# Kernel tuning notes

Measured on AMD Instinct MI355X. Metric: run time of the kernel, lower is better.

Reference implementation:

```python
import jax, jax.numpy as jnp
import numpy as np

def setup_inputs() -> dict:
    key = jax.random.key(0)
    ks = jax.random.split(key, 6)
    B, H, Dk, Dv = 128, 16, 128, 128
    return {
        "q": jax.random.normal(ks[0], (B, H, 1, Dk), dtype=jnp.float32),
        "k": jax.random.normal(ks[1], (B, H, 1, Dk), dtype=jnp.float32),
        "v": jax.random.normal(ks[2], (B, H, 1, Dv), dtype=jnp.float32),
        "g": jax.random.uniform(ks[3], (B, H, 1), dtype=jnp.float32),
        "beta": jax.random.uniform(ks[4], (B, H, 1), dtype=jnp.float32),
        "last_recurrent_state": jax.random.normal(ks[5], (B, H, Dk, Dv), dtype=jnp.float32),
    }

def reference(q, k, v, g, beta, last_recurrent_state):
    # q,k: (B,H,1,Dk); v: (B,H,1,Dv); g,beta: (B,H,1); state: (B,H,Dk,Dv)
    q_t = q[:, :, 0, :]                      # (B,H,Dk)
    k_t = k[:, :, 0, :]                      # (B,H,Dk)
    v_t = v[:, :, 0, :]                      # (B,H,Dv)
    decay = jnp.exp(g)[..., None]            # (B,H,1,1)
    state = last_recurrent_state * decay     # (B,H,Dk,Dv)
    kv_mem = jnp.einsum('bhkv,bhk->bhv', state, k_t)   # (B,H,Dv)
    delta = (v_t - kv_mem) * beta            # (B,H,Dv)
    state = state + k_t[..., :, None] * delta[..., None, :]  # outer update
    out = jnp.einsum('bhkv,bhk->bhv', state, q_t)       # (B,H,Dv)
    out = out[:, :, None, :]                 # (B,H,1,Dv)
    return jnp.concatenate([out.reshape(-1), state.reshape(-1)], axis=0)
```

## Files before the change

kernel.cpp:

```cpp
#include <hip/hip_runtime.h>


#define DK 128
#define DV 128
typedef float f4 __attribute__((ext_vector_type(4)));

__global__ __launch_bounds__(256) void s1_cell_kernel(
    const float* __restrict__ q,
    const float* __restrict__ k,
    const float* __restrict__ v,
    const float* __restrict__ g,
    const float* __restrict__ beta,
    const float* __restrict__ S,
    float* __restrict__ out,
    int BH)
{
    const int bh   = blockIdx.x;
    const int w    = threadIdx.x >> 6;
    const int lane = threadIdx.x & 63;
    const int half = lane >> 5;
    const int c0   = (lane & 31) * 4;

    __shared__ float apart[4][DV];
    __shared__ float bpart[4][DV];
    __shared__ float skq[4];

    const size_t stile = (size_t)bh * (DK * DV);
    const float* __restrict__ Sb = S + stile;
    float* __restrict__ oS = out + (size_t)BH * DV + stile;

    const int r0 = 32 * w + half;

    f4 s[16];
    #pragma unroll
    for (int i = 0; i < 16; ++i)
        s[i] = *(const f4*)(Sb + (size_t)(r0 + 2 * i) * DV + c0);

    float kv[16], qv[16];
    #pragma unroll
    for (int i = 0; i < 16; ++i) {
        kv[i] = k[bh * DK + r0 + 2 * i];
        qv[i] = q[bh * DK + r0 + 2 * i];
    }

    const float decay = expf(g[bh]);
    const float bta   = beta[bh];

    f4 a = {0.f, 0.f, 0.f, 0.f};
    f4 b = {0.f, 0.f, 0.f, 0.f};
    float kqp = 0.f;
    #pragma unroll
    for (int i = 0; i < 16; ++i) {
        a   += s[i] * kv[i];
        b   += s[i] * qv[i];
        kqp += kv[i] * qv[i];
    }

    a.x += __shfl_xor(a.x, 32, 64);  a.y += __shfl_xor(a.y, 32, 64);
    a.z += __shfl_xor(a.z, 32, 64);  a.w += __shfl_xor(a.w, 32, 64);
    b.x += __shfl_xor(b.x, 32, 64);  b.y += __shfl_xor(b.y, 32, 64);
    b.z += __shfl_xor(b.z, 32, 64);  b.w += __shfl_xor(b.w, 32, 64);
    kqp += __shfl_xor(kqp, 32, 64);

    if (lane < 32) {
        *(f4*)&apart[w][c0] = a;
        *(f4*)&bpart[w][c0] = b;
        if (lane == 0) skq[w] = kqp;
    }
    __syncthreads();

    f4 A  = *(const f4*)&apart[0][c0];
    f4 Bq = *(const f4*)&bpart[0][c0];
    #pragma unroll
    for (int j = 1; j < 4; ++j) {
        A  += *(const f4*)&apart[j][c0];
        Bq += *(const f4*)&bpart[j][c0];
    }
    const float kq = skq[0] + skq[1] + skq[2] + skq[3];

    const f4 vv  = *(const f4*)(v + bh * DV + c0);
    const f4 dlt = (vv - decay * A) * bta;

    if (w == 0 && lane < 32)
        *(f4*)(out + (size_t)bh * DV + c0) = decay * Bq + kq * dlt;

    #pragma unroll
    for (int i = 0; i < 16; ++i) {
        const f4 wr = decay * s[i] + kv[i] * dlt;
        __builtin_nontemporal_store(wr,
            (f4*)(oS + (size_t)(r0 + 2 * i) * DV + c0));
    }
}

extern "C" void kernel_launch(void* const* d_in, const int* in_sizes, int n_in,
                              void* d_out, int out_size, void* d_ws, size_t ws_size,
                              hipStream_t stream) {
    const float* q    = (const float*)d_in[0];
    const float* k    = (const float*)d_in[1];
    const float* v    = (const float*)d_in[2];
    const float* g    = (const float*)d_in[3];
    const float* beta = (const float*)d_in[4];
    const float* S    = (const float*)d_in[5];
    float* out = (float*)d_out;

    const int BH = in_sizes[3];

    s1_cell_kernel<<<BH, 256, 0, stream>>>(q, k, v, g, beta, S, out, BH);
}
```

Before: 249.3 us.

## Split fused delta-rule kernel into reduction pass and grid-stride state rewrite

The single per-head kernel is split in two. The first kernel computes the reductions and writes out, delta and decay, saving delta and decay into global scratch arrays. The second kernel is a flat grid-stride streaming kernel that rereads the state and writes the updated state. This decouples the state write from the register-heavy reduction block so the write streams with a simple access pattern. The cost is a second full read of the state, which may be partly served from cache, plus an extra launch and a fixed BH_MAX limit on the scratch buffers.

```diff
diff --git a/kernel.cpp b/kernel.cpp
--- a/kernel.cpp
+++ b/kernel.cpp
@@ -3,17 +3,20 @@
 
 #define DK 128
 #define DV 128
+#define BH_MAX 2048
 typedef float f4 __attribute__((ext_vector_type(4)));
 
-__global__ __launch_bounds__(256) void s1_cell_kernel(
+__device__ float g_delta[BH_MAX * DV];
+__device__ float g_decay[BH_MAX];
+
+__global__ __launch_bounds__(256) void s1_reduce_kernel(
     const float* __restrict__ q,
     const float* __restrict__ k,
     const float* __restrict__ v,
     const float* __restrict__ g,
     const float* __restrict__ beta,
     const float* __restrict__ S,
-    float* __restrict__ out,
-    int BH)
+    float* __restrict__ out)
 {
     const int bh   = blockIdx.x;
     const int w    = threadIdx.x >> 6;
@@ -25,10 +28,7 @@
     __shared__ float bpart[4][DV];
     __shared__ float skq[4];
 
-    const size_t stile = (size_t)bh * (DK * DV);
-    const float* __restrict__ Sb = S + stile;
-    float* __restrict__ oS = out + (size_t)BH * DV + stile;
-
+    const float* __restrict__ Sb = S + (size_t)bh * (DK * DV);
     const int r0 = 32 * w + half;
 
     f4 s[16];
@@ -69,26 +69,46 @@
     }
     __syncthreads();
 
-    f4 A  = *(const f4*)&apart[0][c0];
-    f4 Bq = *(const f4*)&bpart[0][c0];
-    #pragma unroll
-    for (int j = 1; j < 4; ++j) {
-        A  += *(const f4*)&apart[j][c0];
-        Bq += *(const f4*)&bpart[j][c0];
+    if (w == 0 && lane < 32) {
+        f4 A  = *(const f4*)&apart[0][c0];
+        f4 Bq = *(const f4*)&bpart[0][c0];
+        #pragma unroll
+        for (int j = 1; j < 4; ++j) {
+            A  += *(const f4*)&apart[j][c0];
+            Bq += *(const f4*)&bpart[j][c0];
+        }
+        const float kq = skq[0] + skq[1] + skq[2] + skq[3];
+
+        const f4 vv  = *(const f4*)(v + bh * DV + c0);
+        const f4 dlt = (vv - decay * A) * bta;
+
+        *(f4*)(g_delta + (size_t)bh * DV + c0) = dlt;
+        *(f4*)(out + (size_t)bh * DV + c0)     = decay * Bq + kq * dlt;
+        if (lane == 0) g_decay[bh] = decay;
     }
-    const float kq = skq[0] + skq[1] + skq[2] + skq[3];
+}
 
-    const f4 vv  = *(const f4*)(v + bh * DV + c0);
-    const f4 dlt = (vv - decay * A) * bta;
+__global__ __launch_bounds__(256) void s1_rewrite_kernel(
+    const float* __restrict__ k,
+    const float* __restrict__ S,
+    float* __restrict__ outS,
+    size_t total_f4)
+{
+    const size_t stride = (size_t)gridDim.x * blockDim.x;
+    size_t idx = (size_t)blockIdx.x * blockDim.x + threadIdx.x;
 
-    if (w == 0 && lane < 32)
-        *(f4*)(out + (size_t)bh * DV + c0) = decay * Bq + kq * dlt;
+    const int rem = (int)(idx & 4095);
+    const int row = rem >> 5;
+    const int vc  = (rem & 31) * 4;
 
-    #pragma unroll
-    for (int i = 0; i < 16; ++i) {
-        const f4 wr = decay * s[i] + kv[i] * dlt;
-        __builtin_nontemporal_store(wr,
-            (f4*)(oS + (size_t)(r0 + 2 * i) * DV + c0));
+    for (; idx < total_f4; idx += stride) {
+        const int bh = (int)(idx >> 12);
+        const f4    s   = *(const f4*)(S + (idx << 2));
+        const float dec = g_decay[bh];
+        const float kvv = k[bh * DK + row];
+        const f4    dlt = *(const f4*)(g_delta + (size_t)bh * DV + vc);
+        __builtin_nontemporal_store(dec * s + kvv * dlt,
+                                    (f4*)(outS + (idx << 2)));
     }
 }
 
@@ -105,5 +125,10 @@
 
     const int BH = in_sizes[3];
 
-    s1_cell_kernel<<<BH, 256, 0, stream>>>(q, k, v, g, beta, S, out, BH);
+    s1_reduce_kernel<<<BH, 256, 0, stream>>>(q, k, v, g, beta, S, out);
+
+    const size_t total_f4 = (size_t)BH * (DK * DV / 4);
+    s1_rewrite_kernel<<<4096, 256, 0, stream>>>(k, S,
+                                                out + (size_t)BH * DV,
+                                                total_f4);
 }
```

Result: slower. 261.9 us (+5.0%).

## Process two heads per block, prefetching second state tile during first writeback

Applied to the files above, without the earlier changes.

Each block now handles two (batch,head) tiles, with the grid halved. The second tile's state is loaded before the first tile's results are written back, so the load overlaps the store. State loads become nontemporal and the state stores switch from nontemporal to regular. This doubles register pressure (two 16xf4 arrays), which may lower occupancy, and it adds an extra barrier.

```diff
diff --git a/kernel.cpp b/kernel.cpp
--- a/kernel.cpp
+++ b/kernel.cpp
@@ -15,53 +15,49 @@
     float* __restrict__ out,
     int BH)
 {
-    const int bh   = blockIdx.x;
     const int w    = threadIdx.x >> 6;
     const int lane = threadIdx.x & 63;
     const int half = lane >> 5;
     const int c0   = (lane & 31) * 4;
+    const int r0   = 32 * w + half;
 
     __shared__ float apart[4][DV];
     __shared__ float bpart[4][DV];
     __shared__ float skq[4];
 
-    const size_t stile = (size_t)bh * (DK * DV);
-    const float* __restrict__ Sb = S + stile;
-    float* __restrict__ oS = out + (size_t)BH * DV + stile;
+    const int bh0 = blockIdx.x;
+    const int bh1 = blockIdx.x + gridDim.x;
 
-    const int r0 = 32 * w + half;
-
-    f4 s[16];
+    const float* __restrict__ Sb0 = S + (size_t)bh0 * (DK * DV);
+    f4 s0[16];
     #pragma unroll
     for (int i = 0; i < 16; ++i)
-        s[i] = *(const f4*)(Sb + (size_t)(r0 + 2 * i) * DV + c0);
+        s0[i] = __builtin_nontemporal_load(
+                    (const f4*)(Sb0 + (size_t)(r0 + 2 * i) * DV + c0));
 
-    float kv[16], qv[16];
+    float kv0[16];
     #pragma unroll
-    for (int i = 0; i < 16; ++i) {
-        kv[i] = k[bh * DK + r0 + 2 * i];
-        qv[i] = q[bh * DK + r0 + 2 * i];
-    }
+    for (int i = 0; i < 16; ++i)
+        kv0[i] = k[bh0 * DK + r0 + 2 * i];
 
-    const float decay = expf(g[bh]);
-    const float bta   = beta[bh];
+    const float dec0 = expf(g[bh0]);
+    const float bt0  = beta[bh0];
 
     f4 a = {0.f, 0.f, 0.f, 0.f};
     f4 b = {0.f, 0.f, 0.f, 0.f};
     float kqp = 0.f;
     #pragma unroll
     for (int i = 0; i < 16; ++i) {
-        a   += s[i] * kv[i];
-        b   += s[i] * qv[i];
-        kqp += kv[i] * qv[i];
+        const float qv = q[bh0 * DK + r0 + 2 * i];
+        a   += s0[i] * kv0[i];
+        b   += s0[i] * qv;
+        kqp += kv0[i] * qv;
     }
-
     a.x += __shfl_xor(a.x, 32, 64);  a.y += __shfl_xor(a.y, 32, 64);
     a.z += __shfl_xor(a.z, 32, 64);  a.w += __shfl_xor(a.w, 32, 64);
     b.x += __shfl_xor(b.x, 32, 64);  b.y += __shfl_xor(b.y, 32, 64);
     b.z += __shfl_xor(b.z, 32, 64);  b.w += __shfl_xor(b.w, 32, 64);
     kqp += __shfl_xor(kqp, 32, 64);
-
     if (lane < 32) {
         *(f4*)&apart[w][c0] = a;
         *(f4*)&bpart[w][c0] = b;
@@ -76,20 +72,80 @@
         A  += *(const f4*)&apart[j][c0];
         Bq += *(const f4*)&bpart[j][c0];
     }
-    const float kq = skq[0] + skq[1] + skq[2] + skq[3];
+    const float kq0 = skq[0] + skq[1] + skq[2] + skq[3];
+    const f4 vv0  = *(const f4*)(v + bh0 * DV + c0);
+    const f4 dlt0 = (vv0 - dec0 * A) * bt0;
+    if (w == 0 && lane < 32)
+        *(f4*)(out + (size_t)bh0 * DV + c0) = dec0 * Bq + kq0 * dlt0;
 
-    const f4 vv  = *(const f4*)(v + bh * DV + c0);
-    const f4 dlt = (vv - decay * A) * bta;
+    const bool has1 = (bh1 < BH);
+    const float* __restrict__ Sb1 = S + (size_t)bh1 * (DK * DV);
+    f4 s1[16];
+    if (has1) {
+        #pragma unroll
+        for (int i = 0; i < 16; ++i)
+            s1[i] = __builtin_nontemporal_load(
+                        (const f4*)(Sb1 + (size_t)(r0 + 2 * i) * DV + c0));
+    }
 
-    if (w == 0 && lane < 32)
-        *(f4*)(out + (size_t)bh * DV + c0) = decay * Bq + kq * dlt;
+    float* __restrict__ oS0 = out + (size_t)BH * DV + (size_t)bh0 * (DK * DV);
+    #pragma unroll
+    for (int i = 0; i < 16; ++i)
+        *(f4*)(oS0 + (size_t)(r0 + 2 * i) * DV + c0)
+            = dec0 * s0[i] + kv0[i] * dlt0;
 
+    if (!has1) return;
+
+    float kv1[16];
+    #pragma unroll
+    for (int i = 0; i < 16; ++i)
+        kv1[i] = k[bh1 * DK + r0 + 2 * i];
+
+    const float dec1 = expf(g[bh1]);
+    const float bt1  = beta[bh1];
+
+    a = (f4){0.f, 0.f, 0.f, 0.f};
+    b = (f4){0.f, 0.f, 0.f, 0.f};
+    kqp = 0.f;
     #pragma unroll
     for (int i = 0; i < 16; ++i) {
-        const f4 wr = decay * s[i] + kv[i] * dlt;
-        __builtin_nontemporal_store(wr,
-            (f4*)(oS + (size_t)(r0 + 2 * i) * DV + c0));
+        const float qv = q[bh1 * DK + r0 + 2 * i];
+        a   += s1[i] * kv1[i];
+        b   += s1[i] * qv;
+        kqp += kv1[i] * qv;
     }
+    a.x += __shfl_xor(a.x, 32, 64);  a.y += __shfl_xor(a.y, 32, 64);
+    a.z += __shfl_xor(a.z, 32, 64);  a.w += __shfl_xor(a.w, 32, 64);
+    b.x += __shfl_xor(b.x, 32, 64);  b.y += __shfl_xor(b.y, 32, 64);
+    b.z += __shfl_xor(b.z, 32, 64);  b.w += __shfl_xor(b.w, 32, 64);
+    kqp += __shfl_xor(kqp, 32, 64);
+
+    __syncthreads();
+    if (lane < 32) {
+        *(f4*)&apart[w][c0] = a;
+        *(f4*)&bpart[w][c0] = b;
+        if (lane == 0) skq[w] = kqp;
+    }
+    __syncthreads();
+
+    A  = *(const f4*)&apart[0][c0];
+    Bq = *(const f4*)&bpart[0][c0];
+    #pragma unroll
+    for (int j = 1; j < 4; ++j) {
+        A  += *(const f4*)&apart[j][c0];
+        Bq += *(const f4*)&bpart[j][c0];
+    }
+    const float kq1 = skq[0] + skq[1] + skq[2] + skq[3];
+    const f4 vv1  = *(const f4*)(v + bh1 * DV + c0);
+    const f4 dlt1 = (vv1 - dec1 * A) * bt1;
+    if (w == 0 && lane < 32)
+        *(f4*)(out + (size_t)bh1 * DV + c0) = dec1 * Bq + kq1 * dlt1;
+
+    float* __restrict__ oS1 = out + (size_t)BH * DV + (size_t)bh1 * (DK * DV);
+    #pragma unroll
+    for (int i = 0; i < 16; ++i)
+        *(f4*)(oS1 + (size_t)(r0 + 2 * i) * DV + c0)
+            = dec1 * s1[i] + kv1[i] * dlt1;
 }
 
 extern "C" void kernel_launch(void* const* d_in, const int* in_sizes, int n_in,
@@ -105,5 +161,6 @@
 
     const int BH = in_sizes[3];
 
-    s1_cell_kernel<<<BH, 256, 0, stream>>>(q, k, v, g, beta, S, out, BH);
+    const int nblk = (BH + 1) / 2;
+    s1_cell_kernel<<<nblk, 256, 0, stream>>>(q, k, v, g, beta, S, out, BH);
 }
```

Result: faster. 239.5 us (-3.9%).
